# Kernel tuning notes

Measured on AMD Instinct MI355X. Metric: run time of the kernel, lower is better.

## Reference

```python
import jax, jax.numpy as jnp
import numpy as np

MAX_CACHE_LEN = 1024
B, S, D, H = 8, 512, 512, 8
DK = D // H


def setup_inputs() -> dict:
    key = jax.random.key(0)
    ks = jax.random.split(key, 11)
    w = lambda k: jax.random.normal(k, (D, D), jnp.float32) * 0.02
    b = lambda k: jax.random.normal(k, (D,), jnp.float32) * 0.02
    return {
        "x": jax.random.normal(ks[0], (B, S, D), jnp.float32),
        "prev_k": jax.random.normal(ks[1], (B, H, MAX_CACHE_LEN, DK), jnp.float32),
        "prev_v": jax.random.normal(ks[2], (B, H, MAX_CACHE_LEN, DK), jnp.float32),
        "Wq": w(ks[3]), "bq": b(ks[4]),
        "Wk": w(ks[5]), "bk": b(ks[6]),
        "Wv": w(ks[7]), "bv": b(ks[8]),
        "Wo": w(ks[9]), "bo": b(ks[10]),
        "offset": MAX_CACHE_LEN,  # cache already full (steady-state streaming)
    }


def reference(x, prev_k, prev_v, Wq, bq, Wk, bk, Wv, bv, Wo, bo, offset):
    Bx, Sx, Dx = x.shape
    Hx = prev_k.shape[1]
    dk = Dx // Hx
    # projections (torch Linear: y = x @ W.T + b), split into heads -> [B,H,S,dk]
    def proj(W, bias):
        return (x @ W.T + bias).reshape(Bx, Sx, Hx, dk).transpose(0, 2, 1, 3)
    q = proj(Wq, bq)
    k = jnp.concatenate([prev_k, proj(Wk, bk)], axis=2)
    v = jnp.concatenate([prev_v, proj(Wv, bv)], axis=2)
    # sliding-window narrow to last MAX_CACHE_LEN keys (static shapes under jit)
    k_full = k.shape[2]
    start = max(0, k_full - MAX_CACHE_LEN)
    k = k[:, :, start:, :]
    v = v[:, :, start:, :]
    k_len = k.shape[2]
    new_offset = min(offset + Sx, MAX_CACHE_LEN)
    # scores [B,H,S,k_len]
    scores = jnp.einsum("bhqd,bhkd->bhqk", q, k) * (dk ** -0.5)
    q_start = new_offset - Sx
    q_idx = jnp.arange(Sx)[:, None] + q_start
    k_idx = jnp.arange(k_len)[None, :]
    mask = q_idx < k_idx  # future keys masked
    scores = jnp.where(mask[None, None], -jnp.inf, scores)
    attn = jax.nn.softmax(scores, axis=-1)
    out = jnp.einsum("bhqk,bhkd->bhqd", attn, v)
    out = out.transpose(0, 2, 1, 3).reshape(Bx, Sx, Dx)
    out = out @ Wo.T + bo
    return out, k, v, jnp.asarray(new_offset, jnp.int64 if jax.config.x64_enabled else jnp.int32)
```

## Files before the change

kernel.cpp:

```cpp
#include <hip/hip_runtime.h>
#include <math.h>

#define B_  8
#define S_  512
#define D_  512
#define H_  8
#define DK_ 64
#define KL_ 1024

typedef __attribute__((ext_vector_type(8))) short bf16x8;
typedef __attribute__((ext_vector_type(4))) float f32x4;

__device__ __forceinline__ unsigned short f2bf(float f) {
    unsigned u = __float_as_uint(f);
    u += 0x7FFF + ((u >> 16) & 1);
    return (unsigned short)(u >> 16);
}
__device__ __forceinline__ void gld16(const void* g, void* l) {
    __builtin_amdgcn_global_load_lds(
        (const __attribute__((address_space(1))) unsigned int*)g,
        (__attribute__((address_space(3))) unsigned int*)l, 16, 0, 0);
}

__global__ __launch_bounds__(256)
void prep_kernel(const float* __restrict__ x,
                 const float* __restrict__ Wq, const float* __restrict__ Wk,
                 const float* __restrict__ Wv, const float* __restrict__ Wo,
                 unsigned short* __restrict__ xb,
                 unsigned short* __restrict__ Wqb, unsigned short* __restrict__ Wkb,
                 unsigned short* __restrict__ Wvb, unsigned short* __restrict__ Wob,
                 float* __restrict__ off_out) {
    const int blk = blockIdx.x, t = threadIdx.x;
    if (blk == 0 && t == 0) off_out[0] = 1024.0f;

    const float* src; unsigned short* dst; int off;
    if (blk < 1024) {
        src = x; dst = xb; off = blk * 256 + t;
    } else {
        int widx = blk - 1024;
        int grp = widx >> 7, wb = widx & 127;
        const float* ws_[4]        = {Wq, Wk, Wv, Wo};
        unsigned short* wd_[4]     = {Wqb, Wkb, Wvb, Wob};
        src = ws_[grp]; dst = wd_[grp]; off = wb * 256 + t;
    }
    float4 v0 = ((const float4*)src)[off * 2];
    float4 v1 = ((const float4*)src)[off * 2 + 1];
    unsigned short tmp[8] = {f2bf(v0.x), f2bf(v0.y), f2bf(v0.z), f2bf(v0.w),
                             f2bf(v1.x), f2bf(v1.y), f2bf(v1.z), f2bf(v1.w)};
    *(uint4*)&dst[off * 8] = *(uint4*)tmp;
}

__device__ __forceinline__
void prev_copy_body(const float* __restrict__ pk, const float* __restrict__ pv,
                    float* __restrict__ kout, float* __restrict__ vout,
                    unsigned short* __restrict__ Kp, unsigned short* __restrict__ Vp,
                    unsigned char* __restrict__ smem, int pb) {
    float (*Kl)[68] = (float (*)[68])smem;
    float (*Vl)[68] = (float (*)[68])(smem + 17408);
    const int t = threadIdx.x;
    const int kt = pb & 7, bh = pb >> 3;
    const float* Kg = pk + (bh * KL_ + 512 + kt * 64) * DK_;
    const float* Vg = pv + (bh * KL_ + 512 + kt * 64) * DK_;
    float* Ko = kout + (bh * KL_ + kt * 64) * DK_;
    float* Vo = vout + (bh * KL_ + kt * 64) * DK_;
    #pragma unroll
    for (int it = 0; it < 4; ++it) {
        int idx = t + it * 256;
        int row = idx >> 4, c4 = idx & 15;
        float4 kv = *(const float4*)&Kg[row * 64 + c4 * 4];
        float4 vv = *(const float4*)&Vg[row * 64 + c4 * 4];
        *(float4*)&Ko[row * 64 + c4 * 4] = kv;
        *(float4*)&Vo[row * 64 + c4 * 4] = vv;
        *(float4*)&Kl[row][c4 * 4] = kv;
        *(float4*)&Vl[row][c4 * 4] = vv;
    }
    __syncthreads();
    unsigned short* Kpb = Kp + (bh * 16 + kt) * 4096;
    unsigned short* Vpb = Vp + (bh * 16 + kt) * 4096;
    #pragma unroll
    for (int s = 0; s < 2; ++s) {
        int slot = t + s * 256;
        int c = slot >> 6, l = slot & 63;
        int nn = c >> 1, hf = c & 1;
        {
            int row = nn * 16 + (l & 15), col = hf * 32 + (l >> 4) * 8;
            unsigned short tmp[8];
            #pragma unroll
            for (int j = 0; j < 8; ++j) tmp[j] = f2bf(Kl[row][col + j]);
            *(uint4*)&Kpb[c * 512 + l * 8] = *(uint4*)tmp;
        }
        {
            int row0 = hf * 32 + (l >> 4) * 8, col = nn * 16 + (l & 15);
            unsigned short tmp[8];
            #pragma unroll
            for (int j = 0; j < 8; ++j) tmp[j] = f2bf(Vl[row0 + j][col]);
            *(uint4*)&Vpb[c * 512 + l * 8] = *(uint4*)tmp;
        }
    }
    __syncthreads();
}

template<int MODE, int BM>
__device__ __forceinline__
void mfma_gemm_body(const unsigned short* __restrict__ A,
                    const unsigned short* __restrict__ Wb,
                    const float* __restrict__ bias,
                    float* __restrict__ C32, unsigned short* __restrict__ C16,
                    unsigned short* __restrict__ Pk,
                    unsigned char* __restrict__ smem) {
    constexpr int MM = BM / 32;
    unsigned short* As = (unsigned short*)smem;
    unsigned short* Bs = (unsigned short*)(smem + BM * 64);
    const int t = threadIdx.x, l = t & 63, w = t >> 6;
    const int m16 = l & 15, quad = l >> 4;
    const int wm = w >> 1, wn = w & 1;
    const int bn = blockIdx.x, bm = blockIdx.y;
    const int lr = l >> 2, lc = (l & 3) * 8;

    f32x4 acc[MM][2] = {};
    const unsigned short* Ag = A + (bm * BM) * 512;
    const unsigned short* Wg = Wb + (bn * 64) * 512;

    for (int k0 = 0; k0 < 512; k0 += 32) {
        __syncthreads();
        #pragma unroll
        for (int q = 0; q < BM / 64; ++q) {
            int chunk = w * (BM / 64) + q;
            gld16(Ag + (chunk * 16 + lr) * 512 + k0 + lc, &As[chunk * 512 + l * 8]);
        }
        gld16(Wg + (w * 16 + lr) * 512 + k0 + lc, &Bs[w * 512 + l * 8]);
        __syncthreads();

        bf16x8 af[MM], bfr[2];
        #pragma unroll
        for (int mm = 0; mm < MM; ++mm)
            af[mm] = *(const bf16x8*)&As[(wm * (BM / 2) + mm * 16 + m16) * 32 + quad * 8];
        #pragma unroll
        for (int nn = 0; nn < 2; ++nn)
            bfr[nn] = *(const bf16x8*)&Bs[(wn * 32 + nn * 16 + m16) * 32 + quad * 8];
        #pragma unroll
        for (int mm = 0; mm < MM; ++mm)
            #pragma unroll
            for (int nn = 0; nn < 2; ++nn)
                acc[mm][nn] = __builtin_amdgcn_mfma_f32_16x16x32_bf16(
                    af[mm], bfr[nn], acc[mm][nn], 0, 0, 0);
    }

    if constexpr (MODE == 2 || MODE == 4) {
        unsigned short* Ts = (unsigned short*)(smem + BM * 64 + 4096);
        #pragma unroll
        for (int mm = 0; mm < MM; ++mm)
            #pragma unroll
            for (int nn = 0; nn < 2; ++nn) {
                int n = bn * 64 + wn * 32 + nn * 16 + m16;
                float bv_ = bias[n];
                int d = n & 63;
                #pragma unroll
                for (int r = 0; r < 4; ++r) {
                    int ml = wm * (BM / 2) + mm * 16 + quad * 4 + r;
                    int m = bm * BM + ml;
                    float val = acc[mm][nn][r] + bv_;
                    int b = m >> 9, s = m & 511, h = n >> 6;
                    C32[((b * H_ + h) * KL_ + 512 + s) * DK_ + d] = val;
                    if (MODE == 2) Ts[ml * 72 + d]  = f2bf(val);
                    else           Ts[d * 136 + ml] = f2bf(val);
                }
            }
        __syncthreads();
        const int bh = (bm >> 2) * H_ + bn;
        const int kt0 = 8 + (bm & 3) * 2;
        #pragma unroll
        for (int T = 0; T < 2; ++T)
            #pragma unroll
            for (int cp = 0; cp < 2; ++cp) {
                int c = w * 2 + cp, nn = c >> 1, hf = c & 1;
                uint4 frag;
                if (MODE == 2)
                    frag = *(const uint4*)&Ts[(T * 64 + nn * 16 + (l & 15)) * 72
                                              + hf * 32 + (l >> 4) * 8];
                else
                    frag = *(const uint4*)&Ts[(nn * 16 + (l & 15)) * 136
                                              + T * 64 + hf * 32 + (l >> 4) * 8];
                *(uint4*)&Pk[((bh * 16 + kt0 + T) * 4096) + c * 512 + l * 8] = frag;
            }
    } else {
        #pragma unroll
        for (int mm = 0; mm < MM; ++mm)
            #pragma unroll
            for (int nn = 0; nn < 2; ++nn) {
                int n = bn * 64 + wn * 32 + nn * 16 + m16;
                float bv_ = bias[n];
                #pragma unroll
                for (int r = 0; r < 4; ++r) {
                    int m = bm * BM + wm * (BM / 2) + mm * 16 + quad * 4 + r;
                    float val = acc[mm][nn][r] + bv_;
                    if (MODE == 3) {
                        C32[m * 512 + n] = val;
                    } else {
                        int b = m >> 9, s = m & 511;
                        int h = n >> 6, d = n & 63;
                        C16[((b * H_ + h) * S_ + s) * DK_ + d] =
                            f2bf(val * 0.18033688011112042f);
                    }
                }
            }
    }
}

__global__ __launch_bounds__(256, 4)
void qkv_mfma_kernel(const unsigned short* __restrict__ xb,
                     const unsigned short* __restrict__ Wqb, const float* __restrict__ bq,
                     const unsigned short* __restrict__ Wkb, const float* __restrict__ bk,
                     const unsigned short* __restrict__ Wvb, const float* __restrict__ bv,
                     unsigned short* __restrict__ Qb, float* __restrict__ kout,
                     float* __restrict__ vout,
                     unsigned short* __restrict__ Kp, unsigned short* __restrict__ Vp,
                     const float* __restrict__ pk, const float* __restrict__ pv) {
    __shared__ __attribute__((aligned(16))) unsigned char smem[34816];
    if (blockIdx.z == 0)      mfma_gemm_body<1, 128>(xb, Wqb, bq, nullptr, Qb, nullptr, smem);
    else if (blockIdx.z == 1) mfma_gemm_body<2, 128>(xb, Wkb, bk, kout, nullptr, Kp, smem);
    else if (blockIdx.z == 2) mfma_gemm_body<4, 128>(xb, Wvb, bv, vout, nullptr, Vp, smem);
    else {
        int pb0 = blockIdx.y * 8 + blockIdx.x;
        prev_copy_body(pk, pv, kout, vout, Kp, Vp, smem, pb0);
        prev_copy_body(pk, pv, kout, vout, Kp, Vp, smem, pb0 + 256);
    }
}

__global__ __launch_bounds__(256, 4)
void out_mfma_kernel(const unsigned short* __restrict__ Ob, const unsigned short* __restrict__ Wob,
                     const float* __restrict__ bo, float* __restrict__ C) {
    __shared__ __attribute__((aligned(16))) unsigned char smem[8192];
    mfma_gemm_body<3, 64>(Ob, Wob, bo, C, nullptr, nullptr, smem);
}

__global__ __launch_bounds__(128)
void attn_kernel(const unsigned short* __restrict__ Qb,
                 const unsigned short* __restrict__ Kp,
                 const unsigned short* __restrict__ Vp,
                 unsigned short* __restrict__ Ob) {
    const int bh = blockIdx.x, qg = blockIdx.y;
    const int t = threadIdx.x, l = t & 63, w = t >> 6;
    const int m16 = l & 15, quad = l >> 4;
    const int q0 = qg * 32;

    __shared__ __attribute__((aligned(16))) unsigned short Ps[2][32][72];
    __shared__ float comb[64][40];

    bf16x8 qf[2][2];
    #pragma unroll
    for (int qh = 0; qh < 2; ++qh)
        #pragma unroll
        for (int p = 0; p < 2; ++p)
            qf[qh][p] = *(const bf16x8*)(Qb + (bh * S_ + q0 + qh * 16 + m16) * DK_
                                            + p * 32 + quad * 8);

    f32x4 acc[2][4] = {};
    float psum[2][4] = {};

    const int ktmax = (543 + q0) >> 6;
    const unsigned short* Kpb = Kp + (bh * 16) * 4096;
    const unsigned short* Vpb = Vp + (bh * 16) * 4096;

    for (int kt = w; kt <= ktmax; kt += 2) {
        const unsigned short* kb = Kpb + kt * 4096;
        const unsigned short* vb = Vpb + kt * 4096;
        bf16x8 kf[4][2];
        #pragma unroll
        for (int nn = 0; nn < 4; ++nn)
            #pragma unroll
            for (int hf = 0; hf < 2; ++hf)
                kf[nn][hf] = *(const bf16x8*)(kb + ((nn * 2 + hf) * 64 + l) * 8);

        f32x4 sc[2][4];
        #pragma unroll
        for (int qh = 0; qh < 2; ++qh)
            #pragma unroll
            for (int nn = 0; nn < 4; ++nn) {
                sc[qh][nn][0] = sc[qh][nn][1] = sc[qh][nn][2] = sc[qh][nn][3] = 0.f;
                sc[qh][nn] = __builtin_amdgcn_mfma_f32_16x16x32_bf16(qf[qh][0], kf[nn][0], sc[qh][nn], 0, 0, 0);
                sc[qh][nn] = __builtin_amdgcn_mfma_f32_16x16x32_bf16(qf[qh][1], kf[nn][1], sc[qh][nn], 0, 0, 0);
            }

        bf16x8 vf[4][2];
        #pragma unroll
        for (int nn = 0; nn < 4; ++nn)
            #pragma unroll
            for (int hf = 0; hf < 2; ++hf)
                vf[nn][hf] = *(const bf16x8*)(vb + ((nn * 2 + hf) * 64 + l) * 8);

        if (kt == ktmax) {
            #pragma unroll
            for (int qh = 0; qh < 2; ++qh)
                #pragma unroll
                for (int nn = 0; nn < 4; ++nn) {
                    int key = kt * 64 + nn * 16 + m16;
                    #pragma unroll
                    for (int r = 0; r < 4; ++r)
                        if (key > 512 + q0 + qh * 16 + (quad << 2) + r)
                            sc[qh][nn][r] = -INFINITY;
                }
        }

        #pragma unroll
        for (int qh = 0; qh < 2; ++qh)
            #pragma unroll
            for (int nn = 0; nn < 4; ++nn)
                #pragma unroll
                for (int r = 0; r < 4; ++r) {
                    float p = exp2f(sc[qh][nn][r]);
                    psum[qh][r] += p;
                    Ps[w][qh * 16 + (quad << 2) + r][nn * 16 + m16] = f2bf(p);
                }

        bf16x8 pf[2][2];
        #pragma unroll
        for (int qh = 0; qh < 2; ++qh)
            #pragma unroll
            for (int hf = 0; hf < 2; ++hf)
                pf[qh][hf] = *(const bf16x8*)&Ps[w][qh * 16 + m16][hf * 32 + quad * 8];
        #pragma unroll
        for (int qh = 0; qh < 2; ++qh)
            #pragma unroll
            for (int nn = 0; nn < 4; ++nn) {
                acc[qh][nn] = __builtin_amdgcn_mfma_f32_16x16x32_bf16(pf[qh][0], vf[nn][0], acc[qh][nn], 0, 0, 0);
                acc[qh][nn] = __builtin_amdgcn_mfma_f32_16x16x32_bf16(pf[qh][1], vf[nn][1], acc[qh][nn], 0, 0, 0);
            }
    }

    if (w == 0) {
        #pragma unroll
        for (int qh = 0; qh < 2; ++qh)
            #pragma unroll
            for (int nn = 0; nn < 4; ++nn)
                #pragma unroll
                for (int r = 0; r < 4; ++r)
                    comb[l][(qh * 4 + nn) * 4 + r] = acc[qh][nn][r];
        #pragma unroll
        for (int qh = 0; qh < 2; ++qh)
            #pragma unroll
            for (int r = 0; r < 4; ++r)
                comb[l][32 + qh * 4 + r] = psum[qh][r];
    }
    __syncthreads();
    if (w == 1) {
        #pragma unroll
        for (int qh = 0; qh < 2; ++qh)
            #pragma unroll
            for (int nn = 0; nn < 4; ++nn)
                #pragma unroll
                for (int r = 0; r < 4; ++r)
                    acc[qh][nn][r] += comb[l][(qh * 4 + nn) * 4 + r];
        float inv[2][4];
        #pragma unroll
        for (int qh = 0; qh < 2; ++qh)
            #pragma unroll
            for (int r = 0; r < 4; ++r) {
                float ps = psum[qh][r] + comb[l][32 + qh * 4 + r];
                ps += __shfl_xor(ps, 1);
                ps += __shfl_xor(ps, 2);
                ps += __shfl_xor(ps, 4);
                ps += __shfl_xor(ps, 8);
                inv[qh][r] = 1.f / ps;
            }
        unsigned short* Og = Ob + ((bh >> 3) * S_ + q0) * D_ + (bh & 7) * DK_;
        #pragma unroll
        for (int qh = 0; qh < 2; ++qh)
            #pragma unroll
            for (int r = 0; r < 4; ++r)
                #pragma unroll
                for (int nn = 0; nn < 4; ++nn)
                    Og[(qh * 16 + (quad << 2) + r) * D_ + nn * 16 + m16] =
                        f2bf(acc[qh][nn][r] * inv[qh][r]);
    }
}

extern "C" void kernel_launch(void* const* d_in, const int* in_sizes, int n_in,
                              void* d_out, int out_size, void* d_ws, size_t ws_size,
                              hipStream_t stream) {
    const float* x  = (const float*)d_in[0];
    const float* pk = (const float*)d_in[1];
    const float* pv = (const float*)d_in[2];
    const float* Wq = (const float*)d_in[3];
    const float* bq = (const float*)d_in[4];
    const float* Wk = (const float*)d_in[5];
    const float* bk = (const float*)d_in[6];
    const float* Wv = (const float*)d_in[7];
    const float* bv = (const float*)d_in[8];
    const float* Wo = (const float*)d_in[9];
    const float* bo = (const float*)d_in[10];

    float* out     = (float*)d_out;
    float* kout    = out + 2097152;
    float* vout    = kout + 4194304;
    float* off_out = vout + 4194304;

    unsigned short* xb  = (unsigned short*)d_ws;
    unsigned short* Wqb = xb + 2097152;
    unsigned short* Wkb = Wqb + 262144;
    unsigned short* Wvb = Wkb + 262144;
    unsigned short* Wob = Wvb + 262144;
    unsigned short* Qb  = Wob + 262144;
    unsigned short* Kp  = Qb + 2097152;
    unsigned short* Vp  = Kp + 4194304;
    unsigned short* Ob  = xb;

    prep_kernel<<<1536, 256, 0, stream>>>(x, Wq, Wk, Wv, Wo,
                                          xb, Wqb, Wkb, Wvb, Wob, off_out);
    qkv_mfma_kernel<<<dim3(8, 32, 4), 256, 0, stream>>>(xb, Wqb, bq, Wkb, bk, Wvb, bv,
                                                        Qb, kout, vout, Kp, Vp, pk, pv);
    attn_kernel<<<dim3(64, 16), 128, 0, stream>>>(Qb, Kp, Vp, Ob);
    out_mfma_kernel<<<dim3(8, 64), 256, 0, stream>>>(Ob, Wob, bo, out);
}
```

Before: 156.5 us.

## Double-buffer GEMM LDS staging, add MFMA priority hints, reorder block roles

The shared GEMM body now uses two LDS buffers, prefetching the next k-slice with global_load_lds while computing on the current one. This replaces the two barriers per iteration with a single one. The epilogue transpose buffer reuses the start of shared memory, and the output kernel's shared allocation doubles. Attention MFMA sections are wrapped in s_setprio hints, the bf16 conversion now uses the HIP intrinsic, and the prev-cache copy blocks are moved to z=0 so they are dispatched first. Risks include higher LDS use, which may lower occupancy, and possible prefetch/compute races if the async loads are not waited on properly.

```diff
diff --git a/kernel.cpp b/kernel.cpp
--- a/kernel.cpp
+++ b/kernel.cpp
@@ -1,4 +1,5 @@
 #include <hip/hip_runtime.h>
+#include <hip/hip_bf16.h>
 #include <math.h>
 
 #define B_  8
@@ -12,9 +13,10 @@
 typedef __attribute__((ext_vector_type(4))) float f32x4;
 
 __device__ __forceinline__ unsigned short f2bf(float f) {
-    unsigned u = __float_as_uint(f);
-    u += 0x7FFF + ((u >> 16) & 1);
-    return (unsigned short)(u >> 16);
+    __hip_bfloat16 h = __float2bfloat16(f);
+    unsigned short u;
+    __builtin_memcpy(&u, &h, 2);
+    return u;
 }
 __device__ __forceinline__ void gld16(const void* g, void* l) {
     __builtin_amdgcn_global_load_lds(
@@ -109,8 +111,7 @@
                     unsigned short* __restrict__ Pk,
                     unsigned char* __restrict__ smem) {
     constexpr int MM = BM / 32;
-    unsigned short* As = (unsigned short*)smem;
-    unsigned short* Bs = (unsigned short*)(smem + BM * 64);
+    constexpr int ABUF = BM * 64;
     const int t = threadIdx.x, l = t & 63, w = t >> 6;
     const int m16 = l & 15, quad = l >> 4;
     const int wm = w >> 1, wn = w & 1;
@@ -121,33 +122,45 @@
     const unsigned short* Ag = A + (bm * BM) * 512;
     const unsigned short* Wg = Wb + (bn * 64) * 512;
 
-    for (int k0 = 0; k0 < 512; k0 += 32) {
-        __syncthreads();
+    auto stage = [&](int buf, int k0) {
+        unsigned short* Asb = (unsigned short*)(smem + buf * ABUF);
+        unsigned short* Bsb = (unsigned short*)(smem + 2 * ABUF + buf * 4096);
         #pragma unroll
         for (int q = 0; q < BM / 64; ++q) {
             int chunk = w * (BM / 64) + q;
-            gld16(Ag + (chunk * 16 + lr) * 512 + k0 + lc, &As[chunk * 512 + l * 8]);
+            gld16(Ag + (chunk * 16 + lr) * 512 + k0 + lc, &Asb[chunk * 512 + l * 8]);
         }
-        gld16(Wg + (w * 16 + lr) * 512 + k0 + lc, &Bs[w * 512 + l * 8]);
-        __syncthreads();
-
+        gld16(Wg + (w * 16 + lr) * 512 + k0 + lc, &Bsb[w * 512 + l * 8]);
+    };
+
+    stage(0, 0);
+    __syncthreads();
+    int buf = 0;
+    for (int it = 0; it < 16; ++it) {
+        if (it < 15) stage(buf ^ 1, (it + 1) * 32);
+
+        const unsigned short* Asb = (const unsigned short*)(smem + buf * ABUF);
+        const unsigned short* Bsb = (const unsigned short*)(smem + 2 * ABUF + buf * 4096);
         bf16x8 af[MM], bfr[2];
         #pragma unroll
         for (int mm = 0; mm < MM; ++mm)
-            af[mm] = *(const bf16x8*)&As[(wm * (BM / 2) + mm * 16 + m16) * 32 + quad * 8];
+            af[mm] = *(const bf16x8*)&Asb[(wm * (BM / 2) + mm * 16 + m16) * 32 + quad * 8];
         #pragma unroll
         for (int nn = 0; nn < 2; ++nn)
-            bfr[nn] = *(const bf16x8*)&Bs[(wn * 32 + nn * 16 + m16) * 32 + quad * 8];
+            bfr[nn] = *(const bf16x8*)&Bsb[(wn * 32 + nn * 16 + m16) * 32 + quad * 8];
         #pragma unroll
         for (int mm = 0; mm < MM; ++mm)
             #pragma unroll
             for (int nn = 0; nn < 2; ++nn)
                 acc[mm][nn] = __builtin_amdgcn_mfma_f32_16x16x32_bf16(
                     af[mm], bfr[nn], acc[mm][nn], 0, 0, 0);
+
+        __syncthreads();
+        buf ^= 1;
     }
 
     if constexpr (MODE == 2 || MODE == 4) {
-        unsigned short* Ts = (unsigned short*)(smem + BM * 64 + 4096);
+        unsigned short* Ts = (unsigned short*)smem;
         #pragma unroll
         for (int mm = 0; mm < MM; ++mm)
             #pragma unroll
@@ -217,20 +230,20 @@
                      unsigned short* __restrict__ Kp, unsigned short* __restrict__ Vp,
                      const float* __restrict__ pk, const float* __restrict__ pv) {
     __shared__ __attribute__((aligned(16))) unsigned char smem[34816];
-    if (blockIdx.z == 0)      mfma_gemm_body<1, 128>(xb, Wqb, bq, nullptr, Qb, nullptr, smem);
-    else if (blockIdx.z == 1) mfma_gemm_body<2, 128>(xb, Wkb, bk, kout, nullptr, Kp, smem);
-    else if (blockIdx.z == 2) mfma_gemm_body<4, 128>(xb, Wvb, bv, vout, nullptr, Vp, smem);
-    else {
+    if (blockIdx.z == 0) {
         int pb0 = blockIdx.y * 8 + blockIdx.x;
         prev_copy_body(pk, pv, kout, vout, Kp, Vp, smem, pb0);
         prev_copy_body(pk, pv, kout, vout, Kp, Vp, smem, pb0 + 256);
     }
+    else if (blockIdx.z == 1) mfma_gemm_body<1, 128>(xb, Wqb, bq, nullptr, Qb, nullptr, smem);
+    else if (blockIdx.z == 2) mfma_gemm_body<2, 128>(xb, Wkb, bk, kout, nullptr, Kp, smem);
+    else                      mfma_gemm_body<4, 128>(xb, Wvb, bv, vout, nullptr, Vp, smem);
 }
 
 __global__ __launch_bounds__(256, 4)
 void out_mfma_kernel(const unsigned short* __restrict__ Ob, const unsigned short* __restrict__ Wob,
                      const float* __restrict__ bo, float* __restrict__ C) {
-    __shared__ __attribute__((aligned(16))) unsigned char smem[8192];
+    __shared__ __attribute__((aligned(16))) unsigned char smem[16384];
     mfma_gemm_body<3, 64>(Ob, Wob, bo, C, nullptr, nullptr, smem);
 }
 
@@ -273,6 +286,7 @@
                 kf[nn][hf] = *(const bf16x8*)(kb + ((nn * 2 + hf) * 64 + l) * 8);
 
         f32x4 sc[2][4];
+        __builtin_amdgcn_s_setprio(1);
         #pragma unroll
         for (int qh = 0; qh < 2; ++qh)
             #pragma unroll
@@ -281,6 +295,7 @@
                 sc[qh][nn] = __builtin_amdgcn_mfma_f32_16x16x32_bf16(qf[qh][0], kf[nn][0], sc[qh][nn], 0, 0, 0);
                 sc[qh][nn] = __builtin_amdgcn_mfma_f32_16x16x32_bf16(qf[qh][1], kf[nn][1], sc[qh][nn], 0, 0, 0);
             }
+        __builtin_amdgcn_s_setprio(0);
 
         bf16x8 vf[4][2];
         #pragma unroll
@@ -319,6 +334,7 @@
             #pragma unroll
             for (int hf = 0; hf < 2; ++hf)
                 pf[qh][hf] = *(const bf16x8*)&Ps[w][qh * 16 + m16][hf * 32 + quad * 8];
+        __builtin_amdgcn_s_setprio(1);
         #pragma unroll
         for (int qh = 0; qh < 2; ++qh)
             #pragma unroll
@@ -326,6 +342,7 @@
                 acc[qh][nn] = __builtin_amdgcn_mfma_f32_16x16x32_bf16(pf[qh][0], vf[nn][0], acc[qh][nn], 0, 0, 0);
                 acc[qh][nn] = __builtin_amdgcn_mfma_f32_16x16x32_bf16(pf[qh][1], vf[nn][1], acc[qh][nn], 0, 0, 0);
             }
+        __builtin_amdgcn_s_setprio(0);
     }
 
     if (w == 0) {
```

Result: no change. 155.0 us (-1.0%).
